# Performance work log

Measured on AMD Instinct MI355X. Metric: run time of the kernel, lower is better.

## Reference

```python
import jax, jax.numpy as jnp
import numpy as np

B, T, DMODEL = 2, 2048, 1024
H, DK, DV = 16, 64, 64
FF = 4096
EPS = 1e-5


def _layernorm_2d(x):
    # torch LayerNorm(normalized_shape=(T, dmodel)): normalize jointly over last two
    # dims, biased variance, weight=1 / bias=0 (freshly constructed each forward).
    mu = jnp.mean(x, axis=(1, 2), keepdims=True)
    var = jnp.mean((x - mu) ** 2, axis=(1, 2), keepdims=True)
    return (x - mu) / jnp.sqrt(var + EPS)


def setup_inputs() -> dict:
    key = jax.random.key(0)
    ks = jax.random.split(key, 9)
    s = 0.02  # small init for numerical sanity (original uses uniform(-1,1))
    return {
        "x": jax.random.normal(ks[0], (B, T, DMODEL), jnp.float32),
        "Wq": jax.random.normal(ks[1], (H, DMODEL, DK), jnp.float32) * s,
        "Wk": jax.random.normal(ks[2], (H, DMODEL, DK), jnp.float32) * s,
        "Wv": jax.random.normal(ks[3], (H, DMODEL, DV), jnp.float32) * s,
        "Wo": jax.random.normal(ks[4], (DMODEL, DMODEL), jnp.float32) * s,
        "W1": jax.random.normal(ks[5], (DMODEL, FF), jnp.float32) * s,
        "b1": jnp.zeros((FF,), jnp.float32),
        "W2": jax.random.normal(ks[6], (FF, DMODEL), jnp.float32) * s,
        "b2": jnp.zeros((DMODEL,), jnp.float32),
    }


def reference(x, Wq, Wk, Wv, Wo, W1, b1, W2, b2):
    b, t, d = x.shape
    h, _, dk = Wq.shape
    dv = Wv.shape[-1]
    # per-head projections: (B,H,T,dk/dv)
    Qp = jnp.einsum("btd,hdk->bhtk", x, Wq)
    Kp = jnp.einsum("btd,hdk->bhtk", x, Wk)
    Vp = jnp.einsum("btd,hdv->bhtv", x, Wv)
    scores = jnp.einsum("bhqk,bhsk->bhqs", Qp, Kp) / np.sqrt(dk).astype(np.float32)
    # NOTE: original does torch.softmax(heads, 2) -> softmax over the QUERY axis
    attn = jax.nn.softmax(scores, axis=2)
    heads = jnp.einsum("bhqs,bhsv->bqhv", attn, Vp).reshape(b, t, h * dv)
    att_out = heads @ Wo
    o1 = _layernorm_2d(x + att_out)
    ff = jnp.maximum(o1 @ W1 + b1, 0.0) @ W2 + b2
    return _layernorm_2d(o1 + ff)
```

## Files before the change

kernel.cpp:

```cpp
#include <hip/hip_runtime.h>
#include <hip/hip_bf16.h>
#include <cstddef>
#include <cstdint>

typedef __hip_bfloat16 hbf;
typedef __attribute__((ext_vector_type(8))) __bf16 bf16x8;
typedef __attribute__((ext_vector_type(4))) float f32x4;

#define B_ 2
#define T_ 2048
#define D_ 1024
#define H_ 16
#define FF_ 4096
#define EPS_ 1e-5f
#define SCALE_ 0.125f

__device__ __forceinline__ float bf2f(hbf v) { return __bfloat162float(v); }
__device__ __forceinline__ float ldin(const void* p, size_t i, int isbf) {
  return isbf ? __bfloat162float(((const hbf*)p)[i]) : ((const float*)p)[i];
}
__device__ __forceinline__ void ston(void* p, size_t i, float v, int isbf) {
  if (isbf) ((hbf*)p)[i] = __float2bfloat16(v);
  else ((float*)p)[i] = v;
}
__device__ __forceinline__ f32x4 mfma16(bf16x8 a, bf16x8 b, f32x4 c) {
  return __builtin_amdgcn_mfma_f32_16x16x32_bf16(a, b, c, 0, 0, 0);
}
__device__ __forceinline__ bf16x8 ldfrag(const hbf* p) {
  return *(const bf16x8*)p;
}
__device__ __forceinline__ void glds16(const hbf* g, hbf* l) {
  __builtin_amdgcn_global_load_lds(
      (const __attribute__((address_space(1))) void*)g,
      (__attribute__((address_space(3))) void*)l, 16, 0, 0);
}

__global__ __launch_bounds__(256) void detect_dtype(const unsigned* x,
                                                    int* flag) {
  __shared__ int cnt[256];
  int c = 0;
  for (int i = threadIdx.x; i < 4096; i += 256) {
    unsigned low = x[i] & 0xFFFFu;
    unsigned e = (low >> 7) & 0xFFu;
    if (e >= 100u && e <= 142u) c++;
  }
  cnt[threadIdx.x] = c;
  __syncthreads();
  for (int off = 128; off > 0; off >>= 1) {
    if ((int)threadIdx.x < off) cnt[threadIdx.x] += cnt[threadIdx.x + off];
    __syncthreads();
  }
  if (threadIdx.x == 0) *flag = (cnt[0] > 2458) ? 1 : 0;
}

__device__ __forceinline__ void tr_tile(const void* __restrict__ src,
                                        hbf* __restrict__ dst, int R, int C,
                                        size_t zoff, int cx, int ry, int f,
                                        float (*tile)[33]) {
  const int tx = threadIdx.x & 31, ty = threadIdx.x >> 5;
  const int c0 = cx * 32, r0 = ry * 32;
#pragma unroll
  for (int p = 0; p < 4; p++) {
    int rr = p * 8 + ty;
    tile[rr][tx] = ldin(src, zoff + (size_t)(r0 + rr) * C + c0 + tx, f);
  }
  __syncthreads();
#pragma unroll
  for (int p = 0; p < 4; p++) {
    int cc = p * 8 + ty;
    dst[zoff + (size_t)(c0 + cc) * R + r0 + tx] = __float2bfloat16(tile[tx][cc]);
  }
}

__global__ __launch_bounds__(256) void preconv(
    const void* __restrict__ x, const void* __restrict__ Wq,
    const void* __restrict__ Wk, const void* __restrict__ Wv,
    const void* __restrict__ Wo, const void* __restrict__ W1,
    const void* __restrict__ W2, const void* __restrict__ b1,
    const void* __restrict__ b2, hbf* __restrict__ xb,
    hbf* __restrict__ wqkvt, hbf* __restrict__ wot, hbf* __restrict__ w1t,
    hbf* __restrict__ w2t, hbf* __restrict__ b1b, hbf* __restrict__ b2b,
    const int* __restrict__ flag) {
  __shared__ float tile[32][33];
  const int f = *flag;
  const int bid = blockIdx.x;
  if (bid < 3072) {
    int which = bid >> 10;
    int r = bid & 1023;
    int z = r >> 6, rem = r & 63;
    int ry = rem >> 1, cx = rem & 1;
    const void* src = (which == 0) ? Wq : (which == 1) ? Wk : Wv;
    hbf* dst = wqkvt + (size_t)which * (D_ * D_);
    tr_tile(src, dst, 1024, 64, (size_t)z * 65536, cx, ry, f, tile);
  } else if (bid < 4096) {
    int t = bid - 3072;
    tr_tile(Wo, wot, 1024, 1024, 0, t & 31, t >> 5, f, tile);
  } else if (bid < 8192) {
    int t = bid - 4096;
    tr_tile(W1, w1t, 1024, 4096, 0, t & 127, t >> 7, f, tile);
  } else if (bid < 12288) {
    int t = bid - 8192;
    tr_tile(W2, w2t, 4096, 1024, 0, t & 31, t >> 5, f, tile);
  } else if (bid < 13312) {
    size_t base = (size_t)(bid - 12288) * 4096;
    for (int i = threadIdx.x; i < 4096; i += 256)
      xb[base + i] = __float2bfloat16(ldin(x, base + i, f));
  } else if (bid == 13312) {
    for (int i = threadIdx.x; i < FF_; i += 256)
      b1b[i] = __float2bfloat16(ldin(b1, i, f));
  } else {
    for (int i = threadIdx.x; i < D_; i += 256)
      b2b[i] = __float2bfloat16(ldin(b2, i, f));
  }
}

template <int MODE, int BM, int BN>
__global__ __launch_bounds__(256) void gemm_bt(
    const hbf* __restrict__ A, const hbf* __restrict__ Bt, hbf* __restrict__ C,
    float* __restrict__ Cf0, float* __restrict__ Cf1,
    const hbf* __restrict__ e1, float* __restrict__ red, int M, int N, int K,
    int LDK) {
  constexpr int WM = BM / 2, WN = BN / 2;
  constexpr int IF = WM / 16, JF = WN / 16;
  __shared__ alignas(16) hbf As[BM * 64];
  __shared__ alignas(16) hbf Bs[BN * 64];
  const int tid = threadIdx.x;
  const int wave = tid >> 6, lane = tid & 63;
  const int quad = lane >> 4, l16 = lane & 15;
  const int m0 = blockIdx.y * BM, n0 = blockIdx.x * BN;
  const int mw = (wave >> 1) * WM, nw = (wave & 1) * WN;
  const int srow = tid >> 3;
  const int scol = (tid & 7) * 8;
  const int kbase = (MODE == 4) ? blockIdx.z * K : 0;
  const f32x4 zero = {0.f, 0.f, 0.f, 0.f};
  f32x4 acc[IF][JF];
#pragma unroll
  for (int i = 0; i < IF; i++)
#pragma unroll
    for (int j = 0; j < JF; j++) acc[i][j] = zero;

  const hbf* ga = &A[(size_t)(m0 + srow) * LDK + kbase + scol];
  const hbf* gb = &Bt[(size_t)(n0 + srow) * LDK + kbase + scol];
  hbf* lA = &As[wave * 512];
  hbf* lB = &Bs[wave * 512];

  for (int k0 = 0; k0 < K; k0 += 64) {
#pragma unroll
    for (int c = 0; c < BM / 32; c++)
      glds16(ga + (size_t)(c * 32) * LDK + k0, lA + c * 2048);
#pragma unroll
    for (int c = 0; c < BN / 32; c++)
      glds16(gb + (size_t)(c * 32) * LDK + k0, lB + c * 2048);
    __syncthreads();
    bf16x8 af[2][IF], bfr[2][JF];
#pragma unroll
    for (int h = 0; h < 2; h++) {
#pragma unroll
      for (int i = 0; i < IF; i++)
        af[h][i] = ldfrag(&As[(mw + i * 16 + l16) * 64 + h * 32 + quad * 8]);
#pragma unroll
      for (int j = 0; j < JF; j++)
        bfr[h][j] = ldfrag(&Bs[(nw + j * 16 + l16) * 64 + h * 32 + quad * 8]);
    }
#pragma unroll
    for (int h = 0; h < 2; h++)
#pragma unroll
      for (int i = 0; i < IF; i++)
#pragma unroll
        for (int j = 0; j < JF; j++)
          acc[i][j] = mfma16(af[h][i], bfr[h][j], acc[i][j]);
    __syncthreads();
  }
  float ssum = 0.f, ssq = 0.f;
#pragma unroll
  for (int i = 0; i < IF; i++)
#pragma unroll
    for (int j = 0; j < JF; j++)
#pragma unroll
      for (int r = 0; r < 4; r++) {
        int m = m0 + mw + i * 16 + quad * 4 + r;
        int n = n0 + nw + j * 16 + l16;
        float v = acc[i][j][r];
        if (MODE == 0) {
          int which = n >> 10, n1 = n & 1023;
          int h = n1 >> 6, cc = n1 & 63;
          int b = m >> 11, t = m & (T_ - 1);
          if (which == 0) v *= SCALE_;
          C[(size_t)which * ((size_t)B_ * H_ * T_ * 64) +
            (((size_t)(b * H_ + h)) * T_ + t) * 64 + cc] = __float2bfloat16(v);
        } else if (MODE == 1) {
          hbf hv = __float2bfloat16(v + bf2f(e1[(size_t)m * N + n]));
          C[(size_t)m * N + n] = hv;
          float fv = bf2f(hv);
          ssum += fv;
          ssq += fv * fv;
        } else if (MODE == 2) {
          C[(size_t)m * N + n] = __float2bfloat16(fmaxf(v + bf2f(e1[n]), 0.f));
        } else if (MODE == 4) {
          float* Cf = blockIdx.z ? Cf1 : Cf0;
          Cf[(size_t)m * N + n] = v;
        }
      }
  if (MODE == 1) {
    float* sc = (float*)As;
    sc[tid] = ssum;
    sc[256 + tid] = ssq;
    __syncthreads();
    for (int off = 128; off > 0; off >>= 1) {
      if (tid < off) {
        sc[tid] += sc[tid + off];
        sc[256 + tid] += sc[256 + tid + off];
      }
      __syncthreads();
    }
    if (tid == 0) {
      int b = m0 >> 11;
      atomicAdd(&red[b * 2 + 0], sc[0]);
      atomicAdd(&red[b * 2 + 1], sc[256]);
    }
  }
}

__global__ __launch_bounds__(256) void attn_stats(const hbf* __restrict__ Q,
                                                  const hbf* __restrict__ K,
                                                  const hbf* __restrict__ V,
                                                  hbf* __restrict__ Vt) {
  __shared__ alignas(16) hbf Ks[64 * 72];
  __shared__ alignas(16) hbf Qs[64 * 72];
  __shared__ float sAdj[64];
  const int bh = blockIdx.y;
  const int s0 = blockIdx.x * 64;
  const int tid = threadIdx.x;
  const int wave = tid >> 6, lane = tid & 63;
  const int quad = lane >> 4, l16 = lane & 15;
  const int sw = wave * 16;
  const hbf* Kb = K + (size_t)bh * T_ * 64;
  const hbf* Qb = Q + (size_t)bh * T_ * 64;
  const hbf* Vb = V + (size_t)bh * T_ * 64;
  hbf* Vtb = Vt + (size_t)bh * 64 * T_;
  const int r_ = tid >> 3, c_ = (tid & 7) * 8;
#pragma unroll
  for (int c = 0; c < 2; c++) {
    int row = c * 32 + r_;
    *(float4*)(&Ks[row * 72 + c_]) =
        *(const float4*)(&Kb[(size_t)(s0 + row) * 64 + c_]);
  }
  __syncthreads();
  bf16x8 kf0 = ldfrag(&Ks[(sw + l16) * 72 + quad * 8]);
  bf16x8 kf1 = ldfrag(&Ks[(sw + l16) * 72 + 32 + quad * 8]);
  float m_thr[4], l_thr[4];
#pragma unroll
  for (int r = 0; r < 4; r++) {
    m_thr[r] = -1e30f;
    l_thr[r] = 0.f;
  }
  const f32x4 zero = {0.f, 0.f, 0.f, 0.f};
  for (int qt = 0; qt < T_ / 64; qt++) {
    if (qt) __syncthreads();
#pragma unroll
    for (int c = 0; c < 2; c++) {
      int row = c * 32 + r_;
      *(float4*)(&Qs[row * 72 + c_]) =
          *(const float4*)(&Qb[(size_t)(qt * 64 + row) * 64 + c_]);
    }
    __syncthreads();
    f32x4 acc[4];
#pragma unroll
    for (int j = 0; j < 4; j++) {
      bf16x8 qf0 = ldfrag(&Qs[(j * 16 + l16) * 72 + quad * 8]);
      bf16x8 qf1 = ldfrag(&Qs[(j * 16 + l16) * 72 + 32 + quad * 8]);
      f32x4 a = zero;
      a = mfma16(kf0, qf0, a);
      a = mfma16(kf1, qf1, a);
      acc[j] = a;
    }
#pragma unroll
    for (int r = 0; r < 4; r++) {
      float mt = fmaxf(fmaxf(acc[0][r], acc[1][r]),
                       fmaxf(acc[2][r], acc[3][r]));
      float nm = fmaxf(m_thr[r], mt);
      float s = l_thr[r] * __expf(m_thr[r] - nm);
#pragma unroll
      for (int j = 0; j < 4; j++) s += __expf(acc[j][r] - nm);
      l_thr[r] = s;
      m_thr[r] = nm;
    }
  }
#pragma unroll
  for (int d = 1; d < 16; d <<= 1) {
#pragma unroll
    for (int r = 0; r < 4; r++) {
      float om = __shfl_xor(m_thr[r], d);
      float ol = __shfl_xor(l_thr[r], d);
      float nm = fmaxf(m_thr[r], om);
      l_thr[r] = l_thr[r] * __expf(m_thr[r] - nm) + ol * __expf(om - nm);
      m_thr[r] = nm;
    }
  }
  if (l16 == 0) {
#pragma unroll
    for (int r = 0; r < 4; r++)
      sAdj[sw + quad * 4 + r] = m_thr[r] + __logf(l_thr[r]);
  }
  __syncthreads();
#pragma unroll
  for (int c = 0; c < 2; c++) {
    int e = (c * 256 + tid) * 8;
    int r = e >> 6, col = e & 63;
    union alignas(16) {
      hbf h[8];
      float4 f4;
    } u;
    u.f4 = *(const float4*)(&Vb[(size_t)(s0 + r) * 64 + col]);
    float sc = __expf(-sAdj[r]);
#pragma unroll
    for (int k2 = 0; k2 < 8; k2++)
      u.h[k2] = __float2bfloat16(bf2f(u.h[k2]) * sc);
    *(float4*)(&Ks[r * 72 + col]) = u.f4;
  }
  __syncthreads();
#pragma unroll
  for (int c = 0; c < 2; c++) {
    int e = (c * 256 + tid) * 8;
    int v = e >> 6, tt = e & 63;
    union alignas(16) {
      hbf h[8];
      float4 f4;
    } u;
#pragma unroll
    for (int k2 = 0; k2 < 8; k2++) u.h[k2] = Ks[(tt + k2) * 72 + v];
    *(float4*)(&Vtb[(size_t)v * T_ + s0 + tt]) = u.f4;
  }
}

__global__ __launch_bounds__(256) void attn_apply(const hbf* __restrict__ Q,
                                                  const hbf* __restrict__ K,
                                                  const hbf* __restrict__ Vt,
                                                  hbf* __restrict__ heads) {
  __shared__ alignas(16) hbf Ks[64 * 72];
  __shared__ alignas(16) hbf Vs[64 * 72];
  __shared__ alignas(16) hbf Ps[4 * 32 * 72];
  const int bh = blockIdx.y;
  const int b = bh >> 4, h = bh & 15;
  const int q0 = blockIdx.x * 128;
  const int tid = threadIdx.x;
  const int wave = tid >> 6, lane = tid & 63;
  const int quad = lane >> 4, l16 = lane & 15;
  const int qw = wave * 32;
  const hbf* Qb = Q + (size_t)bh * T_ * 64;
  const hbf* Kb = K + (size_t)bh * T_ * 64;
  const hbf* Vtb = Vt + (size_t)bh * 64 * T_;
  hbf* Pw = &Ps[wave * 32 * 72];
  const int r_ = tid >> 3, c_ = (tid & 7) * 8;
  bf16x8 qf[2][2];
#pragma unroll
  for (int i = 0; i < 2; i++)
#pragma unroll
    for (int hh = 0; hh < 2; hh++)
      qf[i][hh] = *(const bf16x8*)&Qb[(size_t)(q0 + qw + i * 16 + l16) * 64 +
                                      hh * 32 + quad * 8];
  const f32x4 zero = {0.f, 0.f, 0.f, 0.f};
  f32x4 accO[2][4];
#pragma unroll
  for (int i = 0; i < 2; i++)
#pragma unroll
    for (int j = 0; j < 4; j++) accO[i][j] = zero;

  for (int st = 0; st < T_ / 64; st++) {
    if (st) __syncthreads();
#pragma unroll
    for (int c = 0; c < 2; c++) {
      int row = c * 32 + r_;
      *(float4*)(&Ks[row * 72 + c_]) =
          *(const float4*)(&Kb[(size_t)(st * 64 + row) * 64 + c_]);
      *(float4*)(&Vs[row * 72 + c_]) =
          *(const float4*)(&Vtb[(size_t)row * T_ + st * 64 + c_]);
    }
    __syncthreads();
    f32x4 accS[2][4];
#pragma unroll
    for (int j = 0; j < 4; j++) {
      bf16x8 kf0 = ldfrag(&Ks[(j * 16 + l16) * 72 + quad * 8]);
      bf16x8 kf1 = ldfrag(&Ks[(j * 16 + l16) * 72 + 32 + quad * 8]);
#pragma unroll
      for (int i = 0; i < 2; i++) {
        f32x4 a = zero;
        a = mfma16(qf[i][0], kf0, a);
        a = mfma16(qf[i][1], kf1, a);
        accS[i][j] = a;
      }
    }
#pragma unroll
    for (int j = 0; j < 4; j++) {
#pragma unroll
      for (int i = 0; i < 2; i++)
#pragma unroll
        for (int r = 0; r < 4; r++) {
          float p = __expf(accS[i][j][r]);
          Pw[(i * 16 + quad * 4 + r) * 72 + j * 16 + l16] =
              __float2bfloat16(p);
        }
    }
    bf16x8 pf[2][2];
#pragma unroll
    for (int i = 0; i < 2; i++) {
      pf[i][0] = ldfrag(&Pw[(i * 16 + l16) * 72 + quad * 8]);
      pf[i][1] = ldfrag(&Pw[(i * 16 + l16) * 72 + 32 + quad * 8]);
    }
#pragma unroll
    for (int j2 = 0; j2 < 4; j2++) {
      bf16x8 vf0 = ldfrag(&Vs[(j2 * 16 + l16) * 72 + quad * 8]);
      bf16x8 vf1 = ldfrag(&Vs[(j2 * 16 + l16) * 72 + 32 + quad * 8]);
#pragma unroll
      for (int i = 0; i < 2; i++) {
        accO[i][j2] = mfma16(pf[i][0], vf0, accO[i][j2]);
        accO[i][j2] = mfma16(pf[i][1], vf1, accO[i][j2]);
      }
    }
  }
#pragma unroll
  for (int i = 0; i < 2; i++)
#pragma unroll
    for (int j2 = 0; j2 < 4; j2++)
#pragma unroll
      for (int r = 0; r < 4; r++) {
        int q = q0 + qw + i * 16 + quad * 4 + r;
        int v = j2 * 16 + l16;
        heads[((size_t)(b * T_ + q)) * D_ + h * 64 + v] =
            __float2bfloat16(accO[i][j2][r]);
      }
}

__global__ __launch_bounds__(256) void ln_norm(const hbf* __restrict__ src,
                                               const float* __restrict__ red,
                                               void* dst,
                                               const int* __restrict__ flag,
                                               int force_bf) {
  const int isbf = force_bf ? 1 : *flag;
  const float invN = 1.f / (float)(T_ * D_);
  for (size_t i = (size_t)blockIdx.x * 256 + threadIdx.x;
       i < (size_t)B_ * T_ * D_; i += (size_t)gridDim.x * 256) {
    int b = (int)(i >> 21);
    float mu = red[b * 2 + 0] * invN;
    float var = red[b * 2 + 1] * invN - mu * mu;
    ston(dst, i, (bf2f(src[i]) - mu) * rsqrtf(var + EPS_), isbf);
  }
}

__global__ __launch_bounds__(256) void ln2_stats(const float* __restrict__ P0,
                                                 const float* __restrict__ P1,
                                                 const hbf* __restrict__ o1,
                                                 const hbf* __restrict__ b2b,
                                                 float* __restrict__ red) {
  __shared__ float s1[256], s2[256];
  const int b = blockIdx.y;
  const size_t base = (size_t)b * (T_ * D_);
  float sum = 0.f, sq = 0.f;
  for (size_t i = (size_t)blockIdx.x * 256 + threadIdx.x; i < (size_t)T_ * D_;
       i += (size_t)gridDim.x * 256) {
    size_t e = base + i;
    float v = P0[e] + P1[e] + bf2f(b2b[i & (D_ - 1)]) + bf2f(o1[e]);
    sum += v;
    sq += v * v;
  }
  s1[threadIdx.x] = sum;
  s2[threadIdx.x] = sq;
  __syncthreads();
  for (int off = 128; off > 0; off >>= 1) {
    if ((int)threadIdx.x < off) {
      s1[threadIdx.x] += s1[threadIdx.x + off];
      s2[threadIdx.x] += s2[threadIdx.x + off];
    }
    __syncthreads();
  }
  if (threadIdx.x == 0) {
    atomicAdd(&red[b * 2 + 0], s1[0]);
    atomicAdd(&red[b * 2 + 1], s2[0]);
  }
}

__global__ __launch_bounds__(256) void ln2_norm(
    const float* __restrict__ P0, const float* __restrict__ P1,
    const hbf* __restrict__ o1, const hbf* __restrict__ b2b,
    const float* __restrict__ red, void* dst, const int* __restrict__ flag) {
  const int isbf = *flag;
  const float invN = 1.f / (float)(T_ * D_);
  for (size_t i = (size_t)blockIdx.x * 256 + threadIdx.x;
       i < (size_t)B_ * T_ * D_; i += (size_t)gridDim.x * 256) {
    int b = (int)(i >> 21);
    float mu = red[b * 2 + 0] * invN;
    float var = red[b * 2 + 1] * invN - mu * mu;
    float v = P0[i] + P1[i] + bf2f(b2b[i & (D_ - 1)]) + bf2f(o1[i]);
    ston(dst, i, (v - mu) * rsqrtf(var + EPS_), isbf);
  }
}

extern "C" void kernel_launch(void* const* d_in, const int* in_sizes, int n_in,
                              void* d_out, int out_size, void* d_ws,
                              size_t ws_size, hipStream_t stream) {
  const void* x = d_in[0];
  const void* Wq = d_in[1];
  const void* Wk = d_in[2];
  const void* Wv = d_in[3];
  const void* Wo = d_in[4];
  const void* W1 = d_in[5];
  const void* W2 = d_in[7];
  const void* b1 = d_in[6];
  const void* b2 = d_in[8];

  const size_t MB = 1024 * 1024;
  if (ws_size < 89 * MB) return;

  char* w = (char*)d_ws;
  hbf* xb = (hbf*)(w + 0 * MB);
  hbf* wqkvt = (hbf*)(w + 8 * MB);
  hbf* wot = (hbf*)(w + 14 * MB);
  hbf* w1t = (hbf*)(w + 16 * MB);
  hbf* w2t = (hbf*)(w + 24 * MB);
  hbf* Qb = (hbf*)(w + 32 * MB);
  hbf* Kb = (hbf*)(w + 40 * MB);
  hbf* Vb = (hbf*)(w + 48 * MB);
  hbf* Vtb = (hbf*)(w + 56 * MB);
  hbf* heads = (hbf*)(w + 64 * MB);
  hbf* r1 = (hbf*)(w + 72 * MB);
  hbf* o1 = (hbf*)(w + 80 * MB);
  hbf* ff1 = (hbf*)(w + 32 * MB);
  float* P0 = (float*)(w + 0 * MB);
  float* P1 = (float*)(w + 64 * MB);
  hbf* b1b = (hbf*)(w + 88 * MB);
  hbf* b2b = b1b + FF_;
  float* red = (float*)(b2b + D_);
  int* flag = (int*)(red + 8);

  hipMemsetAsync(red, 0, 8 * sizeof(float) + sizeof(int), stream);
  detect_dtype<<<1, 256, 0, stream>>>((const unsigned*)x, flag);

  const int M = B_ * T_;
  preconv<<<13314, 256, 0, stream>>>(x, Wq, Wk, Wv, Wo, W1, W2, b1, b2, xb,
                                     wqkvt, wot, w1t, w2t, b1b, b2b, flag);
  gemm_bt<0, 128, 128><<<dim3(24, 32), 256, 0, stream>>>(
      xb, wqkvt, Qb, nullptr, nullptr, nullptr, nullptr, M, 3 * D_, D_, D_);
  attn_stats<<<dim3(32, 32), 256, 0, stream>>>(Qb, Kb, Vb, Vtb);
  attn_apply<<<dim3(16, 32), 256, 0, stream>>>(Qb, Kb, Vtb, heads);
  gemm_bt<1, 128, 64><<<dim3(16, 32), 256, 0, stream>>>(
      heads, wot, r1, nullptr, nullptr, xb, red, M, D_, D_, D_);
  ln_norm<<<4096, 256, 0, stream>>>(r1, red, o1, flag, 1);
  gemm_bt<2, 128, 128><<<dim3(32, 32), 256, 0, stream>>>(
      o1, w1t, ff1, nullptr, nullptr, b1b, nullptr, M, FF_, D_, D_);
  gemm_bt<4, 128, 128><<<dim3(8, 32, 2), 256, 0, stream>>>(
      ff1, w2t, nullptr, P0, P1, nullptr, nullptr, M, D_, FF_ / 2, FF_);
  ln2_stats<<<dim3(256, B_), 256, 0, stream>>>(P0, P1, o1, b2b, red + 4);
  ln2_norm<<<2048, 256, 0, stream>>>(P0, P1, o1, b2b, red + 4, d_out, flag);
}
```

Measured before the change: 470.7 us.

## Use exp2 with log2e-folded scale and halve attn_apply query tile

Folds log2(e) into the Q scale constant so softmax statistics and probabilities use the native exp2/log2 instructions instead of __expf/__logf. Separately, attn_apply now processes 64 queries per block (16 per wave) instead of 128, doubling the grid to 1024 blocks for better occupancy and CU coverage on the 256-CU device. The trade is that each K/V tile loaded into LDS is reused across half as many queries, doubling K/V global traffic and the LDS staging per unit of work.

```diff
diff --git a/kernel.cpp b/kernel.cpp
--- a/kernel.cpp
+++ b/kernel.cpp
@@ -13,9 +13,15 @@
 #define H_ 16
 #define FF_ 4096
 #define EPS_ 1e-5f
-#define SCALE_ 0.125f
+#define SCALE_ 0.18033688011112f
 
 __device__ __forceinline__ float bf2f(hbf v) { return __bfloat162float(v); }
+__device__ __forceinline__ float fexp2(float x) {
+  return __builtin_amdgcn_exp2f(x);
+}
+__device__ __forceinline__ float flog2(float x) {
+  return __builtin_amdgcn_logf(x);
+}
 __device__ __forceinline__ float ldin(const void* p, size_t i, int isbf) {
   return isbf ? __bfloat162float(((const hbf*)p)[i]) : ((const float*)p)[i];
 }
@@ -279,9 +285,9 @@
       float mt = fmaxf(fmaxf(acc[0][r], acc[1][r]),
                        fmaxf(acc[2][r], acc[3][r]));
       float nm = fmaxf(m_thr[r], mt);
-      float s = l_thr[r] * __expf(m_thr[r] - nm);
-#pragma unroll
-      for (int j = 0; j < 4; j++) s += __expf(acc[j][r] - nm);
+      float s = l_thr[r] * fexp2(m_thr[r] - nm);
+#pragma unroll
+      for (int j = 0; j < 4; j++) s += fexp2(acc[j][r] - nm);
       l_thr[r] = s;
       m_thr[r] = nm;
     }
@@ -293,14 +299,14 @@
       float om = __shfl_xor(m_thr[r], d);
       float ol = __shfl_xor(l_thr[r], d);
       float nm = fmaxf(m_thr[r], om);
-      l_thr[r] = l_thr[r] * __expf(m_thr[r] - nm) + ol * __expf(om - nm);
+      l_thr[r] = l_thr[r] * fexp2(m_thr[r] - nm) + ol * fexp2(om - nm);
       m_thr[r] = nm;
     }
   }
   if (l16 == 0) {
 #pragma unroll
     for (int r = 0; r < 4; r++)
-      sAdj[sw + quad * 4 + r] = m_thr[r] + __logf(l_thr[r]);
+      sAdj[sw + quad * 4 + r] = m_thr[r] + flog2(l_thr[r]);
   }
   __syncthreads();
 #pragma unroll
@@ -312,7 +318,7 @@
       float4 f4;
     } u;
     u.f4 = *(const float4*)(&Vb[(size_t)(s0 + r) * 64 + col]);
-    float sc = __expf(-sAdj[r]);
+    float sc = fexp2(-sAdj[r]);
 #pragma unroll
     for (int k2 = 0; k2 < 8; k2++)
       u.h[k2] = __float2bfloat16(bf2f(u.h[k2]) * sc);
@@ -339,32 +345,28 @@
                                                   hbf* __restrict__ heads) {
   __shared__ alignas(16) hbf Ks[64 * 72];
   __shared__ alignas(16) hbf Vs[64 * 72];
-  __shared__ alignas(16) hbf Ps[4 * 32 * 72];
+  __shared__ alignas(16) hbf Ps[4 * 16 * 72];
   const int bh = blockIdx.y;
   const int b = bh >> 4, h = bh & 15;
-  const int q0 = blockIdx.x * 128;
+  const int q0 = blockIdx.x * 64;
   const int tid = threadIdx.x;
   const int wave = tid >> 6, lane = tid & 63;
   const int quad = lane >> 4, l16 = lane & 15;
-  const int qw = wave * 32;
+  const int qw = wave * 16;
   const hbf* Qb = Q + (size_t)bh * T_ * 64;
   const hbf* Kb = K + (size_t)bh * T_ * 64;
   const hbf* Vtb = Vt + (size_t)bh * 64 * T_;
-  hbf* Pw = &Ps[wave * 32 * 72];
+  hbf* Pw = &Ps[wave * 16 * 72];
   const int r_ = tid >> 3, c_ = (tid & 7) * 8;
-  bf16x8 qf[2][2];
-#pragma unroll
-  for (int i = 0; i < 2; i++)
-#pragma unroll
-    for (int hh = 0; hh < 2; hh++)
-      qf[i][hh] = *(const bf16x8*)&Qb[(size_t)(q0 + qw + i * 16 + l16) * 64 +
-                                      hh * 32 + quad * 8];
+  bf16x8 qf[2];
+#pragma unroll
+  for (int hh = 0; hh < 2; hh++)
+    qf[hh] = *(const bf16x8*)&Qb[(size_t)(q0 + qw + l16) * 64 + hh * 32 +
+                                 quad * 8];
   const f32x4 zero = {0.f, 0.f, 0.f, 0.f};
-  f32x4 accO[2][4];
-#pragma unroll
-  for (int i = 0; i < 2; i++)
-#pragma unroll
-    for (int j = 0; j < 4; j++) accO[i][j] = zero;
+  f32x4 accO[4];
+#pragma unroll
+  for (int j = 0; j < 4; j++) accO[j] = zero;
 
   for (int st = 0; st < T_ / 64; st++) {
     if (st) __syncthreads();
@@ -377,58 +379,44 @@
           *(const float4*)(&Vtb[(size_t)row * T_ + st * 64 + c_]);
     }
     __syncthreads();
-    f32x4 accS[2][4];
+    f32x4 accS[4];
 #pragma unroll
     for (int j = 0; j < 4; j++) {
       bf16x8 kf0 = ldfrag(&Ks[(j * 16 + l16) * 72 + quad * 8]);
       bf16x8 kf1 = ldfrag(&Ks[(j * 16 + l16) * 72 + 32 + quad * 8]);
-#pragma unroll
-      for (int i = 0; i < 2; i++) {
-        f32x4 a = zero;
-        a = mfma16(qf[i][0], kf0, a);
-        a = mfma16(qf[i][1], kf1, a);
-        accS[i][j] = a;
+      f32x4 a = zero;
+      a = mfma16(qf[0], kf0, a);
+      a = mfma16(qf[1], kf1, a);
+      accS[j] = a;
+    }
+#pragma unroll
+    for (int j = 0; j < 4; j++) {
+#pragma unroll
+      for (int r = 0; r < 4; r++) {
+        float p = fexp2(accS[j][r]);
+        Pw[(quad * 4 + r) * 72 + j * 16 + l16] = __float2bfloat16(p);
       }
     }
-#pragma unroll
-    for (int j = 0; j < 4; j++) {
-#pragma unroll
-      for (int i = 0; i < 2; i++)
-#pragma unroll
-        for (int r = 0; r < 4; r++) {
-          float p = __expf(accS[i][j][r]);
-          Pw[(i * 16 + quad * 4 + r) * 72 + j * 16 + l16] =
-              __float2bfloat16(p);
-        }
-    }
-    bf16x8 pf[2][2];
-#pragma unroll
-    for (int i = 0; i < 2; i++) {
-      pf[i][0] = ldfrag(&Pw[(i * 16 + l16) * 72 + quad * 8]);
-      pf[i][1] = ldfrag(&Pw[(i * 16 + l16) * 72 + 32 + quad * 8]);
-    }
+    bf16x8 pf[2];
+    pf[0] = ldfrag(&Pw[l16 * 72 + quad * 8]);
+    pf[1] = ldfrag(&Pw[l16 * 72 + 32 + quad * 8]);
 #pragma unroll
     for (int j2 = 0; j2 < 4; j2++) {
       bf16x8 vf0 = ldfrag(&Vs[(j2 * 16 + l16) * 72 + quad * 8]);
       bf16x8 vf1 = ldfrag(&Vs[(j2 * 16 + l16) * 72 + 32 + quad * 8]);
-#pragma unroll
-      for (int i = 0; i < 2; i++) {
-        accO[i][j2] = mfma16(pf[i][0], vf0, accO[i][j2]);
-        accO[i][j2] = mfma16(pf[i][1], vf1, accO[i][j2]);
-      }
-    }
-  }
-#pragma unroll
-  for (int i = 0; i < 2; i++)
-#pragma unroll
-    for (int j2 = 0; j2 < 4; j2++)
-#pragma unroll
-      for (int r = 0; r < 4; r++) {
-        int q = q0 + qw + i * 16 + quad * 4 + r;
-        int v = j2 * 16 + l16;
-        heads[((size_t)(b * T_ + q)) * D_ + h * 64 + v] =
-            __float2bfloat16(accO[i][j2][r]);
-      }
+      accO[j2] = mfma16(pf[0], vf0, accO[j2]);
+      accO[j2] = mfma16(pf[1], vf1, accO[j2]);
+    }
+  }
+#pragma unroll
+  for (int j2 = 0; j2 < 4; j2++)
+#pragma unroll
+    for (int r = 0; r < 4; r++) {
+      int q = q0 + qw + quad * 4 + r;
+      int v = j2 * 16 + l16;
+      heads[((size_t)(b * T_ + q)) * D_ + h * 64 + v] =
+          __float2bfloat16(accO[j2][r]);
+    }
 }
 
 __global__ __launch_bounds__(256) void ln_norm(const hbf* __restrict__ src,
@@ -541,7 +529,7 @@
   gemm_bt<0, 128, 128><<<dim3(24, 32), 256, 0, stream>>>(
       xb, wqkvt, Qb, nullptr, nullptr, nullptr, nullptr, M, 3 * D_, D_, D_);
   attn_stats<<<dim3(32, 32), 256, 0, stream>>>(Qb, Kb, Vb, Vtb);
-  attn_apply<<<dim3(16, 32), 256, 0, stream>>>(Qb, Kb, Vtb, heads);
+  attn_apply<<<dim3(32, 32), 256, 0, stream>>>(Qb, Kb, Vtb, heads);
   gemm_bt<1, 128, 64><<<dim3(16, 32), 256, 0, stream>>>(
       heads, wot, r1, nullptr, nullptr, xb, red, M, D_, D_, D_);
   ln_norm<<<4096, 256, 0, stream>>>(r1, red, o1, flag, 1);
```

Measured after the change: 480.1 us. No clear change (+2.0%).

## Use exp2 with folded log2e scale and load K/V fragments directly in attention

Applied to the files above, without the earlier changes.

Folds log2(e) into the score scale so the softmax stats and attention apply use hardware exp2/log2 instead of expf/logf. The attention-apply kernel drops the shared K/V staging tiles and block-wide barriers, loading MFMA fragments straight from global memory per wave. The QK product is computed transposed so each lane writes P as packed 4-element stores. This removes two syncs per tile and most LDS traffic, at the cost of redundant global loads of K/V across the four waves, which now rely on cache.

```diff
diff --git a/kernel.cpp b/kernel.cpp
--- a/kernel.cpp
+++ b/kernel.cpp
@@ -13,9 +13,15 @@
 #define H_ 16
 #define FF_ 4096
 #define EPS_ 1e-5f
-#define SCALE_ 0.125f
+#define SCALE_ 0.18033688011112f
 
 __device__ __forceinline__ float bf2f(hbf v) { return __bfloat162float(v); }
+__device__ __forceinline__ float fexp2(float x) {
+  return __builtin_amdgcn_exp2f(x);
+}
+__device__ __forceinline__ float flog2(float x) {
+  return __builtin_amdgcn_logf(x);
+}
 __device__ __forceinline__ float ldin(const void* p, size_t i, int isbf) {
   return isbf ? __bfloat162float(((const hbf*)p)[i]) : ((const float*)p)[i];
 }
@@ -279,9 +285,9 @@
       float mt = fmaxf(fmaxf(acc[0][r], acc[1][r]),
                        fmaxf(acc[2][r], acc[3][r]));
       float nm = fmaxf(m_thr[r], mt);
-      float s = l_thr[r] * __expf(m_thr[r] - nm);
-#pragma unroll
-      for (int j = 0; j < 4; j++) s += __expf(acc[j][r] - nm);
+      float s = l_thr[r] * fexp2(m_thr[r] - nm);
+#pragma unroll
+      for (int j = 0; j < 4; j++) s += fexp2(acc[j][r] - nm);
       l_thr[r] = s;
       m_thr[r] = nm;
     }
@@ -293,14 +299,14 @@
       float om = __shfl_xor(m_thr[r], d);
       float ol = __shfl_xor(l_thr[r], d);
       float nm = fmaxf(m_thr[r], om);
-      l_thr[r] = l_thr[r] * __expf(m_thr[r] - nm) + ol * __expf(om - nm);
+      l_thr[r] = l_thr[r] * fexp2(m_thr[r] - nm) + ol * fexp2(om - nm);
       m_thr[r] = nm;
     }
   }
   if (l16 == 0) {
 #pragma unroll
     for (int r = 0; r < 4; r++)
-      sAdj[sw + quad * 4 + r] = m_thr[r] + __logf(l_thr[r]);
+      sAdj[sw + quad * 4 + r] = m_thr[r] + flog2(l_thr[r]);
   }
   __syncthreads();
 #pragma unroll
@@ -312,7 +318,7 @@
       float4 f4;
     } u;
     u.f4 = *(const float4*)(&Vb[(size_t)(s0 + r) * 64 + col]);
-    float sc = __expf(-sAdj[r]);
+    float sc = fexp2(-sAdj[r]);
 #pragma unroll
     for (int k2 = 0; k2 < 8; k2++)
       u.h[k2] = __float2bfloat16(bf2f(u.h[k2]) * sc);
@@ -337,9 +343,7 @@
                                                   const hbf* __restrict__ K,
                                                   const hbf* __restrict__ Vt,
                                                   hbf* __restrict__ heads) {
-  __shared__ alignas(16) hbf Ks[64 * 72];
-  __shared__ alignas(16) hbf Vs[64 * 72];
-  __shared__ alignas(16) hbf Ps[4 * 32 * 72];
+  __shared__ alignas(16) hbf P2[4 * 2 * 16 * 72];
   const int bh = blockIdx.y;
   const int b = bh >> 4, h = bh & 15;
   const int q0 = blockIdx.x * 128;
@@ -350,16 +354,15 @@
   const hbf* Qb = Q + (size_t)bh * T_ * 64;
   const hbf* Kb = K + (size_t)bh * T_ * 64;
   const hbf* Vtb = Vt + (size_t)bh * 64 * T_;
-  hbf* Pw = &Ps[wave * 32 * 72];
-  const int r_ = tid >> 3, c_ = (tid & 7) * 8;
+  hbf* Pw = &P2[wave * (2 * 16 * 72)];
+  const f32x4 zero = {0.f, 0.f, 0.f, 0.f};
   bf16x8 qf[2][2];
 #pragma unroll
   for (int i = 0; i < 2; i++)
 #pragma unroll
     for (int hh = 0; hh < 2; hh++)
-      qf[i][hh] = *(const bf16x8*)&Qb[(size_t)(q0 + qw + i * 16 + l16) * 64 +
-                                      hh * 32 + quad * 8];
-  const f32x4 zero = {0.f, 0.f, 0.f, 0.f};
+      qf[i][hh] = ldfrag(&Qb[(size_t)(q0 + qw + i * 16 + l16) * 64 + hh * 32 +
+                             quad * 8]);
   f32x4 accO[2][4];
 #pragma unroll
   for (int i = 0; i < 2; i++)
@@ -367,56 +370,54 @@
     for (int j = 0; j < 4; j++) accO[i][j] = zero;
 
   for (int st = 0; st < T_ / 64; st++) {
-    if (st) __syncthreads();
-#pragma unroll
-    for (int c = 0; c < 2; c++) {
-      int row = c * 32 + r_;
-      *(float4*)(&Ks[row * 72 + c_]) =
-          *(const float4*)(&Kb[(size_t)(st * 64 + row) * 64 + c_]);
-      *(float4*)(&Vs[row * 72 + c_]) =
-          *(const float4*)(&Vtb[(size_t)row * T_ + st * 64 + c_]);
-    }
-    __syncthreads();
+    const hbf* Kt = &Kb[(size_t)(st * 64 + l16) * 64 + quad * 8];
+    bf16x8 kf[4][2];
+#pragma unroll
+    for (int j = 0; j < 4; j++)
+#pragma unroll
+      for (int hh = 0; hh < 2; hh++)
+        kf[j][hh] = ldfrag(Kt + j * (16 * 64) + hh * 32);
     f32x4 accS[2][4];
 #pragma unroll
-    for (int j = 0; j < 4; j++) {
-      bf16x8 kf0 = ldfrag(&Ks[(j * 16 + l16) * 72 + quad * 8]);
-      bf16x8 kf1 = ldfrag(&Ks[(j * 16 + l16) * 72 + 32 + quad * 8]);
-#pragma unroll
-      for (int i = 0; i < 2; i++) {
-        f32x4 a = zero;
-        a = mfma16(qf[i][0], kf0, a);
-        a = mfma16(qf[i][1], kf1, a);
-        accS[i][j] = a;
+    for (int i = 0; i < 2; i++)
+#pragma unroll
+      for (int j = 0; j < 4; j++) {
+        f32x4 a = mfma16(kf[j][0], qf[i][0], zero);
+        accS[i][j] = mfma16(kf[j][1], qf[i][1], a);
       }
-    }
-#pragma unroll
-    for (int j = 0; j < 4; j++) {
-#pragma unroll
-      for (int i = 0; i < 2; i++)
-#pragma unroll
-        for (int r = 0; r < 4; r++) {
-          float p = __expf(accS[i][j][r]);
-          Pw[(i * 16 + quad * 4 + r) * 72 + j * 16 + l16] =
-              __float2bfloat16(p);
-        }
-    }
-    bf16x8 pf[2][2];
-#pragma unroll
-    for (int i = 0; i < 2; i++) {
-      pf[i][0] = ldfrag(&Pw[(i * 16 + l16) * 72 + quad * 8]);
-      pf[i][1] = ldfrag(&Pw[(i * 16 + l16) * 72 + 32 + quad * 8]);
-    }
-#pragma unroll
-    for (int j2 = 0; j2 < 4; j2++) {
-      bf16x8 vf0 = ldfrag(&Vs[(j2 * 16 + l16) * 72 + quad * 8]);
-      bf16x8 vf1 = ldfrag(&Vs[(j2 * 16 + l16) * 72 + 32 + quad * 8]);
-#pragma unroll
-      for (int i = 0; i < 2; i++) {
-        accO[i][j2] = mfma16(pf[i][0], vf0, accO[i][j2]);
-        accO[i][j2] = mfma16(pf[i][1], vf1, accO[i][j2]);
+#pragma unroll
+    for (int i = 0; i < 2; i++)
+#pragma unroll
+      for (int j = 0; j < 4; j++) {
+        union {
+          hbf h4[4];
+          uint2 u;
+        } pk;
+#pragma unroll
+        for (int r = 0; r < 4; r++)
+          pk.h4[r] = __float2bfloat16(fexp2(accS[i][j][r]));
+        *(uint2*)&Pw[i * (16 * 72) + l16 * 72 + j * 16 + quad * 4] = pk.u;
       }
-    }
+    bf16x8 pf[2][2], vf[4][2];
+#pragma unroll
+    for (int i = 0; i < 2; i++)
+#pragma unroll
+      for (int hh = 0; hh < 2; hh++)
+        pf[i][hh] =
+            ldfrag(&Pw[i * (16 * 72) + l16 * 72 + hh * 32 + quad * 8]);
+#pragma unroll
+    for (int j2 = 0; j2 < 4; j2++)
+#pragma unroll
+      for (int hh = 0; hh < 2; hh++)
+        vf[j2][hh] = ldfrag(&Vtb[(size_t)(j2 * 16 + l16) * T_ + st * 64 +
+                                 hh * 32 + quad * 8]);
+#pragma unroll
+    for (int i = 0; i < 2; i++)
+#pragma unroll
+      for (int j2 = 0; j2 < 4; j2++) {
+        accO[i][j2] = mfma16(pf[i][0], vf[j2][0], accO[i][j2]);
+        accO[i][j2] = mfma16(pf[i][1], vf[j2][1], accO[i][j2]);
+      }
   }
 #pragma unroll
   for (int i = 0; i < 2; i++)
```

Measured after the change: 528.1 us. 12.2% more time.
